# Optimization experiments

Measured on AMD Instinct MI355X. Metric: run time of the kernel, lower is better.

## Reference

```python
import jax, jax.numpy as jnp
import numpy as np

_EPS = 1e-7  # clamp for BCE numerical validity (torch BCE asserts input in [0,1])


def _erode6(m):
    """Binary erosion with 3D 6-connectivity (scipy generate_binary_structure(3,1)),
    border_value=0. m: [B, C, D, H, W] float in {0,1}. Erosion of a binary mask with
    a cross structuring element == min over the voxel and its 6 face neighbors."""
    p = jnp.pad(m, ((0, 0), (0, 0), (1, 1), (1, 1), (1, 1)))  # zero pad == border_value 0
    e = p[:, :, 1:-1, 1:-1, 1:-1]
    e = jnp.minimum(e, p[:, :, :-2, 1:-1, 1:-1])
    e = jnp.minimum(e, p[:, :, 2:, 1:-1, 1:-1])
    e = jnp.minimum(e, p[:, :, 1:-1, :-2, 1:-1])
    e = jnp.minimum(e, p[:, :, 1:-1, 2:, 1:-1])
    e = jnp.minimum(e, p[:, :, 1:-1, 1:-1, :-2])
    e = jnp.minimum(e, p[:, :, 1:-1, 1:-1, 2:])
    return e


def _boundary_map(mask):
    """Faithful to _get_boundary_map: binarize (astype(bool) == nonzero), erode each
    channel, boundary = float_mask - eroded, sum over channels. Returns [B, D, H, W]."""
    mask = mask.astype(jnp.float32)
    mb = (mask != 0).astype(jnp.float32)
    eroded = _erode6(mb)
    return jnp.sum(mask - eroded, axis=1)


def setup_inputs() -> dict:
    key = jax.random.key(0)
    k1, k2 = jax.random.split(key)
    B, C, D, H, W = 4, 2, 128, 192, 192
    inputs = jax.random.normal(k1, (B, C, D, H, W), dtype=jnp.float32)
    targets = jax.random.randint(k2, (B, C, D, H, W), 0, 2, dtype=jnp.int32)
    return {"inputs": inputs, "targets": targets}


def reference(inputs, targets):
    p = jax.nn.sigmoid(inputs)
    boundary_targets = _boundary_map(targets)
    boundary_inputs = _boundary_map(p)
    # binary_cross_entropy(boundary_inputs, boundary_targets, reduction='none')
    bi = jnp.clip(boundary_inputs, _EPS, 1.0 - _EPS)
    loss = -(boundary_targets * jnp.log(bi) + (1.0 - boundary_targets) * jnp.log1p(-bi))
    return jnp.mean(loss)  # reduction='mean'
```

## Files before the change

### kernel.cpp

```cpp
#include <hip/hip_runtime.h>
#include <math.h>

#define Bq 4
#define Dd 128
#define Hh 192
#define Ww 192

typedef unsigned long long ull;

constexpr int HW    = Hh * Ww;
constexpr int DHW   = Dd * HW;
constexpr int CDHW  = 2 * DHW;
constexpr float INV_N = 1.0f / 18874368.0f;

constexpr int DT = 7,  DSEGN = 18;
constexpr int HT = 19, HSEGN = 10;

#define C0f 1.00000005e-07f
#define C1f 16.1180955f

__device__ __forceinline__ float edge_loss(float x0, float x1, float bt) {
    float p0 = 1.f / (1.f + expf(-x0));
    float p1 = 1.f / (1.f + expf(-x1));
    float bi = fminf(fmaxf(p0 + p1, 1e-7f), 1.f - 1e-7f);
    return -(bt * logf(bi) + (1.f - bt) * log1pf(-bi));
}

__device__ __forceinline__ void block_reduce_atomic(float loss, float* out) {
    #pragma unroll
    for (int off = 32; off > 0; off >>= 1)
        loss += __shfl_down(loss, off, 64);
    __shared__ float s[4];
    int lane = threadIdx.x & 63;
    int wid  = threadIdx.x >> 6;
    if (lane == 0) s[wid] = loss;
    __syncthreads();
    if (threadIdx.x == 0)
        atomicAdd(out, (s[0] + s[1] + s[2] + s[3]) * INV_N);
}

__global__ __launch_bounds__(256) void interior_kernel(
    const float* __restrict__ x,
    const int*   __restrict__ t,
    float*       __restrict__ out)
{
    const int tid  = threadIdx.x;
    const int hseg = blockIdx.x;
    const int dseg = blockIdx.y;
    const int b    = blockIdx.z;
    const int dlo  = 1 + dseg * DT;
    const int hlo  = 1 + hseg * HT;

    __shared__ ull pk[DT + 2][HT + 2][2][3];

    const int wave = tid >> 6, lane = tid & 63;

    for (int rs = wave; rs < (DT + 2) * (HT + 2); rs += 4) {
        int dp = rs / (HT + 2);
        int hp = rs % (HT + 2);
        const int* base = t + b * CDHW + (dlo - 1 + dp) * HW
                            + (hlo - 1 + hp) * Ww + lane;
        int v0 = base[0],       v1 = base[64],       v2 = base[128];
        int v3 = base[DHW],     v4 = base[DHW + 64], v5 = base[DHW + 128];
        ull b0 = __ballot(v0 != 0);
        ull b1 = __ballot(v1 != 0);
        ull b2 = __ballot(v2 != 0);
        ull b3 = __ballot(v3 != 0);
        ull b4 = __ballot(v4 != 0);
        ull b5 = __ballot(v5 != 0);
        if (lane == 0) {
            pk[dp][hp][0][0] = b0; pk[dp][hp][0][1] = b1; pk[dp][hp][0][2] = b2;
            pk[dp][hp][1][0] = b3; pk[dp][hp][1][1] = b4; pk[dp][hp][1][2] = b5;
        }
    }
    __syncthreads();

    float loss = 0.f;
    if (tid < DT * HT) {
        int di = tid / HT, hi = tid % HT;
        int dp = 1 + di,  hp = 1 + hi;
        int d = dlo + di, h = hlo + hi;

        ull c00 = pk[dp][hp][0][0],   c01 = pk[dp][hp][0][1],   c02 = pk[dp][hp][0][2];
        ull c10 = pk[dp][hp][1][0],   c11 = pk[dp][hp][1][1],   c12 = pk[dp][hp][1][2];
        ull n00 = pk[dp][hp-1][0][0], n01 = pk[dp][hp-1][0][1], n02 = pk[dp][hp-1][0][2];
        ull n10 = pk[dp][hp-1][1][0], n11 = pk[dp][hp-1][1][1], n12 = pk[dp][hp-1][1][2];
        ull s00 = pk[dp][hp+1][0][0], s01 = pk[dp][hp+1][0][1], s02 = pk[dp][hp+1][0][2];
        ull s10 = pk[dp][hp+1][1][0], s11 = pk[dp][hp+1][1][1], s12 = pk[dp][hp+1][1][2];
        ull f00 = pk[dp-1][hp][0][0], f01 = pk[dp-1][hp][0][1], f02 = pk[dp-1][hp][0][2];
        ull f10 = pk[dp-1][hp][1][0], f11 = pk[dp-1][hp][1][1], f12 = pk[dp-1][hp][1][2];
        ull k00 = pk[dp+1][hp][0][0], k01 = pk[dp+1][hp][0][1], k02 = pk[dp+1][hp][0][2];
        ull k10 = pk[dp+1][hp][1][0], k11 = pk[dp+1][hp][1][1], k12 = pk[dp+1][hp][1][2];

        ull lm00 = c00 << 1, lm01 = (c01 << 1) | (c00 >> 63), lm02 = (c02 << 1) | (c01 >> 63);
        ull rm00 = (c00 >> 1) | (c01 << 63), rm01 = (c01 >> 1) | (c02 << 63), rm02 = c02 >> 1;
        ull lm10 = c10 << 1, lm11 = (c11 << 1) | (c10 >> 63), lm12 = (c12 << 1) | (c11 >> 63);
        ull rm10 = (c10 >> 1) | (c11 << 63), rm11 = (c11 >> 1) | (c12 << 63), rm12 = c12 >> 1;

        ull e00 = c00 & lm00 & rm00 & n00 & s00 & f00 & k00;
        ull e01 = c01 & lm01 & rm01 & n01 & s01 & f01 & k01;
        ull e02 = c02 & lm02 & rm02 & n02 & s02 & f02 & k02;
        ull e10 = c10 & lm10 & rm10 & n10 & s10 & f10 & k10;
        ull e11 = c11 & lm11 & rm11 & n11 & s11 & f11 & k11;
        ull e12 = c12 & lm12 & rm12 & n12 & s12 & f12 & k12;

        int btsum = __popcll(c00) + __popcll(c01) + __popcll(c02)
                  + __popcll(c10) + __popcll(c11) + __popcll(c12)
                  - __popcll(e00) - __popcll(e01) - __popcll(e02)
                  - __popcll(e10) - __popcll(e11) - __popcll(e12);

        int bt_w0   = (int)(c00 & 1)   + (int)(c10 & 1);
        int bt_w191 = (int)(c02 >> 63) + (int)(c12 >> 63);
        int ibt = btsum - bt_w0 - bt_w191;

        int xb = b * CDHW + d * HW + h * Ww;
        loss = fmaf((float)ibt, C1f, 190.f * C0f)
             + edge_loss(x[xb],       x[xb + DHW],       (float)bt_w0)
             + edge_loss(x[xb + 191], x[xb + DHW + 191], (float)bt_w191);
    }
    block_reduce_atomic(loss, out);
}

constexpr int NF1 = Bq * 2 * Hh * 48;
constexpr int NF2 = Bq * 2 * 126 * 48;
constexpr int NF  = NF1 + NF2;

__global__ __launch_bounds__(256) void face_kernel(
    const float* __restrict__ x, const int* __restrict__ t,
    float* __restrict__ out)
{
    int fid = blockIdx.x * 256 + threadIdx.x;
    float loss = 0.f;
    if (fid < NF) {
        int b, d, h, q;
        if (fid < NF1) {
            q = fid % 48;
            h = (fid / 48) % Hh;
            d = ((fid / (48 * Hh)) & 1) ? Dd - 1 : 0;
            b = fid / (48 * Hh * 2);
        } else {
            int g = fid - NF1;
            q = g % 48;
            d = 1 + (g / 48) % 126;
            h = ((g / (48 * 126)) & 1) ? Hh - 1 : 0;
            b = g / (48 * 126 * 2);
        }
        int v0 = b * CDHW + d * HW + h * Ww + q * 4;
        int4 t0 = *(const int4*)(t + v0);
        int4 t1 = *(const int4*)(t + v0 + DHW);
        float4 xa  = *(const float4*)(x + v0);
        float4 xb4 = *(const float4*)(x + v0 + DHW);
        loss  = edge_loss(xa.x, xb4.x, (float)(t0.x + t1.x));
        loss += edge_loss(xa.y, xb4.y, (float)(t0.y + t1.y));
        loss += edge_loss(xa.z, xb4.z, (float)(t0.z + t1.z));
        loss += edge_loss(xa.w, xb4.w, (float)(t0.w + t1.w));
    }
    block_reduce_atomic(loss, out);
}

extern "C" void kernel_launch(void* const* d_in, const int* in_sizes, int n_in,
                              void* d_out, int out_size, void* d_ws, size_t ws_size,
                              hipStream_t stream) {
    const float* x = (const float*)d_in[0];
    const int*   t = (const int*)d_in[1];
    float* out = (float*)d_out;

    hipMemsetAsync(out, 0, sizeof(float), stream);

    dim3 grid(HSEGN, DSEGN, Bq);
    interior_kernel<<<grid, 256, 0, stream>>>(x, t, out);
    face_kernel<<<(NF + 255) / 256, 256, 0, stream>>>(x, t, out);
}
```

Baseline: 294.7 us.

## Pre-pack targets into bitmask in separate kernel before interior erosion

Adds a pack kernel that streams the int32 targets once and writes a compact bit-packed mask to workspace. The interior kernel then loads its halo tile from the packed words instead of rereading int32 targets with ballots. This removes the halo-overlap rereads of the large target tensor, at the cost of an extra launch and a small intermediate buffer. The packing shifts raw values, so it assumes targets are strictly 0 or 1.

```diff
diff --git a/kernel.cpp b/kernel.cpp
--- a/kernel.cpp
+++ b/kernel.cpp
@@ -11,6 +11,11 @@
 constexpr int HW    = Hh * Ww;
 constexpr int DHW   = Dd * HW;
 constexpr int CDHW  = 2 * DHW;
+constexpr int WPR   = 3;
+constexpr int WPP   = Hh * WPR;
+constexpr int WPC   = Dd * WPP;
+constexpr int TOTW  = Bq * 2 * WPC;
+constexpr int NPKB  = TOTW * 8;
 constexpr float INV_N = 1.0f / 18874368.0f;
 
 constexpr int DT = 7,  DSEGN = 18;
@@ -39,9 +44,23 @@
         atomicAdd(out, (s[0] + s[1] + s[2] + s[3]) * INV_N);
 }
 
+__global__ __launch_bounds__(256) void pack_kernel(
+    const int* __restrict__ t, unsigned char* __restrict__ pk)
+{
+    int i = blockIdx.x * 256 + threadIdx.x;
+    const int4* p = reinterpret_cast<const int4*>(t) + (i << 1);
+    int4 a = p[0];
+    int4 b = p[1];
+    unsigned byte = (unsigned)a.x | ((unsigned)a.y << 1) | ((unsigned)a.z << 2)
+                  | ((unsigned)a.w << 3) | ((unsigned)b.x << 4)
+                  | ((unsigned)b.y << 5) | ((unsigned)b.z << 6)
+                  | ((unsigned)b.w << 7);
+    pk[i] = (unsigned char)byte;
+}
+
 __global__ __launch_bounds__(256) void interior_kernel(
     const float* __restrict__ x,
-    const int*   __restrict__ t,
+    const ull*   __restrict__ pkw,
     float*       __restrict__ out)
 {
     const int tid  = threadIdx.x;
@@ -53,25 +72,15 @@
 
     __shared__ ull pk[DT + 2][HT + 2][2][3];
 
-    const int wave = tid >> 6, lane = tid & 63;
-
-    for (int rs = wave; rs < (DT + 2) * (HT + 2); rs += 4) {
-        int dp = rs / (HT + 2);
-        int hp = rs % (HT + 2);
-        const int* base = t + b * CDHW + (dlo - 1 + dp) * HW
-                            + (hlo - 1 + hp) * Ww + lane;
-        int v0 = base[0],       v1 = base[64],       v2 = base[128];
-        int v3 = base[DHW],     v4 = base[DHW + 64], v5 = base[DHW + 128];
-        ull b0 = __ballot(v0 != 0);
-        ull b1 = __ballot(v1 != 0);
-        ull b2 = __ballot(v2 != 0);
-        ull b3 = __ballot(v3 != 0);
-        ull b4 = __ballot(v4 != 0);
-        ull b5 = __ballot(v5 != 0);
-        if (lane == 0) {
-            pk[dp][hp][0][0] = b0; pk[dp][hp][0][1] = b1; pk[dp][hp][0][2] = b2;
-            pk[dp][hp][1][0] = b3; pk[dp][hp][1][1] = b4; pk[dp][hp][1][2] = b5;
-        }
+    constexpr int NW = (DT + 2) * (HT + 2) * 2 * 3;
+    for (int ws = tid; ws < NW; ws += 256) {
+        int j  = ws % 3;
+        int c  = (ws / 3) & 1;
+        int rp = ws / 6;
+        int hp = rp % (HT + 2);
+        int dp = rp / (HT + 2);
+        pk[dp][hp][c][j] = pkw[(b * 2 + c) * WPC + (dlo - 1 + dp) * WPP
+                               + (hlo - 1 + hp) * WPR + j];
     }
     __syncthreads();
 
@@ -164,10 +173,13 @@
     const float* x = (const float*)d_in[0];
     const int*   t = (const int*)d_in[1];
     float* out = (float*)d_out;
+    unsigned char* pkb = (unsigned char*)d_ws;
+    const ull* pkw = (const ull*)d_ws;
 
     hipMemsetAsync(out, 0, sizeof(float), stream);
 
+    pack_kernel<<<NPKB / 256, 256, 0, stream>>>(t, pkb);
     dim3 grid(HSEGN, DSEGN, Bq);
-    interior_kernel<<<grid, 256, 0, stream>>>(x, t, out);
+    interior_kernel<<<grid, 256, 0, stream>>>(x, pkw, out);
     face_kernel<<<(NF + 255) / 256, 256, 0, stream>>>(x, t, out);
 }
```

After: 292.9 us. Within noise of the previous version (-0.6%).

## Fuse face and interior kernels, unroll halo loads, prefetch edge inputs

Applied to the files above, without the earlier changes.

Merges the interior tile kernel and the face kernel into a single launch, with extra blocks at the end of the grid handling the faces. The halo-loading loop becomes a fixed-trip unrolled loop that clamps the row index, so more global loads can be in flight per wave. The x values for the edge voxels are now loaded before the barrier so their latency overlaps the bit-packing work. The cost is redundant reloads of the last halo row by the clamped iterations and a branchy, larger kernel.

```diff
diff --git a/kernel.cpp b/kernel.cpp
--- a/kernel.cpp
+++ b/kernel.cpp
@@ -15,6 +15,12 @@
 
 constexpr int DT = 7,  DSEGN = 18;
 constexpr int HT = 19, HSEGN = 10;
+constexpr int NTILE = HSEGN * DSEGN * Bq;
+
+constexpr int NF1 = Bq * 2 * Hh * 48;
+constexpr int NF2 = Bq * 2 * 126 * 48;
+constexpr int NF  = NF1 + NF2;
+constexpr int NFBLK = NF / 256;
 
 #define C0f 1.00000005e-07f
 #define C1f 16.1180955f
@@ -39,15 +45,47 @@
         atomicAdd(out, (s[0] + s[1] + s[2] + s[3]) * INV_N);
 }
 
-__global__ __launch_bounds__(256) void interior_kernel(
+__global__ __launch_bounds__(256) void boundary_loss_kernel(
     const float* __restrict__ x,
     const int*   __restrict__ t,
     float*       __restrict__ out)
 {
-    const int tid  = threadIdx.x;
-    const int hseg = blockIdx.x;
-    const int dseg = blockIdx.y;
-    const int b    = blockIdx.z;
+    const int tid = threadIdx.x;
+
+    if (blockIdx.x >= NTILE) {
+        int fid = (blockIdx.x - NTILE) * 256 + tid;
+        float loss = 0.f;
+        {
+            int b, d, h, q;
+            if (fid < NF1) {
+                q = fid % 48;
+                h = (fid / 48) % Hh;
+                d = ((fid / (48 * Hh)) & 1) ? Dd - 1 : 0;
+                b = fid / (48 * Hh * 2);
+            } else {
+                int g = fid - NF1;
+                q = g % 48;
+                d = 1 + (g / 48) % 126;
+                h = ((g / (48 * 126)) & 1) ? Hh - 1 : 0;
+                b = g / (48 * 126 * 2);
+            }
+            int v0 = b * CDHW + d * HW + h * Ww + q * 4;
+            int4 t0 = *(const int4*)(t + v0);
+            int4 t1 = *(const int4*)(t + v0 + DHW);
+            float4 xa  = *(const float4*)(x + v0);
+            float4 xb4 = *(const float4*)(x + v0 + DHW);
+            loss  = edge_loss(xa.x, xb4.x, (float)(t0.x + t1.x));
+            loss += edge_loss(xa.y, xb4.y, (float)(t0.y + t1.y));
+            loss += edge_loss(xa.z, xb4.z, (float)(t0.z + t1.z));
+            loss += edge_loss(xa.w, xb4.w, (float)(t0.w + t1.w));
+        }
+        block_reduce_atomic(loss, out);
+        return;
+    }
+
+    const int hseg = blockIdx.x % HSEGN;
+    const int dseg = (blockIdx.x / HSEGN) % DSEGN;
+    const int b    = blockIdx.x / (HSEGN * DSEGN);
     const int dlo  = 1 + dseg * DT;
     const int hlo  = 1 + hseg * HT;
 
@@ -55,13 +93,16 @@
 
     const int wave = tid >> 6, lane = tid & 63;
 
-    for (int rs = wave; rs < (DT + 2) * (HT + 2); rs += 4) {
+    #pragma unroll 8
+    for (int k = 0; k < 48; ++k) {
+        int rs = wave * 48 + k;
+        if (rs > (DT + 2) * (HT + 2) - 1) rs = (DT + 2) * (HT + 2) - 1;
         int dp = rs / (HT + 2);
         int hp = rs % (HT + 2);
         const int* base = t + b * CDHW + (dlo - 1 + dp) * HW
                             + (hlo - 1 + hp) * Ww + lane;
-        int v0 = base[0],       v1 = base[64],       v2 = base[128];
-        int v3 = base[DHW],     v4 = base[DHW + 64], v5 = base[DHW + 128];
+        int v0 = base[0],   v1 = base[64],       v2 = base[128];
+        int v3 = base[DHW], v4 = base[DHW + 64], v5 = base[DHW + 128];
         ull b0 = __ballot(v0 != 0);
         ull b1 = __ballot(v1 != 0);
         ull b2 = __ballot(v2 != 0);
@@ -73,13 +114,22 @@
             pk[dp][hp][1][0] = b3; pk[dp][hp][1][1] = b4; pk[dp][hp][1][2] = b5;
         }
     }
+
+    float xe0 = 0.f, xe1 = 0.f, xe2 = 0.f, xe3 = 0.f;
+    int d = 0, h = 0;
+    if (tid < DT * HT) {
+        int di = tid / HT, hi = tid % HT;
+        d = dlo + di; h = hlo + hi;
+        int xb = b * CDHW + d * HW + h * Ww;
+        xe0 = x[xb];       xe1 = x[xb + DHW];
+        xe2 = x[xb + 191]; xe3 = x[xb + DHW + 191];
+    }
     __syncthreads();
 
     float loss = 0.f;
     if (tid < DT * HT) {
         int di = tid / HT, hi = tid % HT;
         int dp = 1 + di,  hp = 1 + hi;
-        int d = dlo + di, h = hlo + hi;
 
         ull c00 = pk[dp][hp][0][0],   c01 = pk[dp][hp][0][1],   c02 = pk[dp][hp][0][2];
         ull c10 = pk[dp][hp][1][0],   c11 = pk[dp][hp][1][1],   c12 = pk[dp][hp][1][2];
@@ -113,47 +163,9 @@
         int bt_w191 = (int)(c02 >> 63) + (int)(c12 >> 63);
         int ibt = btsum - bt_w0 - bt_w191;
 
-        int xb = b * CDHW + d * HW + h * Ww;
         loss = fmaf((float)ibt, C1f, 190.f * C0f)
-             + edge_loss(x[xb],       x[xb + DHW],       (float)bt_w0)
-             + edge_loss(x[xb + 191], x[xb + DHW + 191], (float)bt_w191);
-    }
-    block_reduce_atomic(loss, out);
-}
-
-constexpr int NF1 = Bq * 2 * Hh * 48;
-constexpr int NF2 = Bq * 2 * 126 * 48;
-constexpr int NF  = NF1 + NF2;
-
-__global__ __launch_bounds__(256) void face_kernel(
-    const float* __restrict__ x, const int* __restrict__ t,
-    float* __restrict__ out)
-{
-    int fid = blockIdx.x * 256 + threadIdx.x;
-    float loss = 0.f;
-    if (fid < NF) {
-        int b, d, h, q;
-        if (fid < NF1) {
-            q = fid % 48;
-            h = (fid / 48) % Hh;
-            d = ((fid / (48 * Hh)) & 1) ? Dd - 1 : 0;
-            b = fid / (48 * Hh * 2);
-        } else {
-            int g = fid - NF1;
-            q = g % 48;
-            d = 1 + (g / 48) % 126;
-            h = ((g / (48 * 126)) & 1) ? Hh - 1 : 0;
-            b = g / (48 * 126 * 2);
-        }
-        int v0 = b * CDHW + d * HW + h * Ww + q * 4;
-        int4 t0 = *(const int4*)(t + v0);
-        int4 t1 = *(const int4*)(t + v0 + DHW);
-        float4 xa  = *(const float4*)(x + v0);
-        float4 xb4 = *(const float4*)(x + v0 + DHW);
-        loss  = edge_loss(xa.x, xb4.x, (float)(t0.x + t1.x));
-        loss += edge_loss(xa.y, xb4.y, (float)(t0.y + t1.y));
-        loss += edge_loss(xa.z, xb4.z, (float)(t0.z + t1.z));
-        loss += edge_loss(xa.w, xb4.w, (float)(t0.w + t1.w));
+             + edge_loss(xe0, xe1, (float)bt_w0)
+             + edge_loss(xe2, xe3, (float)bt_w191);
     }
     block_reduce_atomic(loss, out);
 }
@@ -167,7 +179,5 @@
 
     hipMemsetAsync(out, 0, sizeof(float), stream);
 
-    dim3 grid(HSEGN, DSEGN, Bq);
-    interior_kernel<<<grid, 256, 0, stream>>>(x, t, out);
-    face_kernel<<<(NF + 255) / 256, 256, 0, stream>>>(x, t, out);
+    boundary_loss_kernel<<<NTILE + NFBLK, 256, 0, stream>>>(x, t, out);
 }
```

Result: faster. 287.6 us (-2.4%).
